# Kernel optimization log

Measured on AMD Instinct MI355X. Metric: run time of the kernel, lower is better.

The kernel has to match this reference:

```python
import jax, jax.numpy as jnp
import numpy as np

B, H, S, D = 2048, 1024, 32768, 64  # batch, hidden_dim, memory_slots, slot_size


def setup_inputs() -> dict:
    key = jax.random.key(0)
    ks = jax.random.split(key, 8)
    inp = {
        "query": jax.random.normal(ks[0], (B, H), jnp.float32),
        "consciousness_level": jax.random.uniform(ks[1], (B,), jnp.float32),
        "content": jax.random.normal(ks[2], (B, H), jnp.float32),
        "memory": jax.random.normal(ks[3], (S, D), jnp.float32) * 0.1,
        "memory_age": jnp.zeros((S,), jnp.float32),
        "memory_strength": jnp.ones((S,), jnp.float32) * 0.1,
        "W_read": jax.random.normal(ks[4], (H + 1, S), jnp.float32) / np.sqrt(H + 1),
        "b_read": jnp.zeros((S,), jnp.float32),
        "W_write": jax.random.normal(ks[5], (H + 1, S), jnp.float32) / np.sqrt(H + 1),
        "b_write": jnp.zeros((S,), jnp.float32),
        "W_cp": jax.random.normal(ks[6], (H, D), jnp.float32) / np.sqrt(H),
        "b_cp": jnp.zeros((D,), jnp.float32),
        "W_ce": jax.random.normal(ks[7], (D, H), jnp.float32) / np.sqrt(D),
        "b_ce": jnp.zeros((H,), jnp.float32),
    }
    return inp


def reference(query, consciousness_level, content, memory, memory_age,
              memory_strength, W_read, b_read, W_write, b_write,
              W_cp, b_cp, W_ce, b_ce):
    # ---- read path ----
    enhanced_query = jnp.concatenate([query, consciousness_level[:, None]], axis=-1)  # [B, H+1]
    read_weights = jax.nn.softmax(enhanced_query @ W_read + b_read, axis=-1)          # [B, S]
    boosted = read_weights * memory_strength[None, :]
    boosted = boosted / (boosted.sum(axis=-1, keepdims=True) + 1e-6)
    read_content = boosted @ memory                                                   # [B, D]
    consciousness_boost = read_content @ W_ce + b_ce                                  # [B, H]

    # ---- write path (vectorized masked consolidation over all slots) ----
    c_mean = consciousness_level.mean()
    write_weights = jax.nn.softmax(enhanced_query @ W_write + b_write, axis=-1)       # [B, S]
    ww_mean = write_weights.mean(axis=0)                                              # [S]
    pc_mean = (content @ W_cp + b_cp).mean(axis=0)                                    # [D]
    weight = ww_mean * (c_mean * 2.0)                                                 # [S]
    gate = c_mean >= 0.3                                                              # auto-activation threshold
    mask = (weight > 0.005) & gate                                                    # [S] bool
    consolidation = jax.nn.sigmoid(memory_age * 0.1 + c_mean)                         # [S]
    alpha = weight * consolidation                                                    # [S]
    new_memory = jnp.where(mask[:, None],
                           (1.0 - alpha)[:, None] * memory + alpha[:, None] * pc_mean[None, :],
                           memory)                                                    # [S, D]
    new_age = memory_age + mask.astype(memory_age.dtype)
    new_strength = jnp.where(mask,
                             jnp.clip(memory_strength + weight * 0.1, 0.1, 2.0),
                             memory_strength)
    return read_content, consciousness_boost, new_memory, new_age, new_strength
```

## Files before the change

kernel.cpp:

```cpp
#include <hip/hip_runtime.h>
#include <hip/hip_bf16.h>
#include <cstdint>
#include <cstddef>

#define B_ 2048
#define H_ 1024
#define S_ 32768
#define D_ 64
#define BT 32
#define KQ 1024
#define NT 16

typedef unsigned char u8;
typedef unsigned short u16;
typedef __attribute__((ext_vector_type(8))) short bf16x8;
typedef __attribute__((ext_vector_type(8))) unsigned short ushort8v;
typedef __attribute__((ext_vector_type(4))) float f32x4;

#define WS_CMEAN      0
#define WS_PCMEAN     64
#define WS_CMM        128
#define WS_ZR         (WS_CMM + H_)
#define WS_TR         (WS_ZR + B_)
#define WS_VR         (WS_TR + B_)
#define WS_ZW         (WS_VR + B_*D_)
#define WS_WWM        (WS_ZW + B_)
#define WS_END        (WS_WWM + S_)

__device__ __forceinline__ u16 f2bf(float f) {
  unsigned u = __float_as_uint(f);
  unsigned r = (u + 0x7FFFu + ((u >> 16) & 1u)) >> 16;
  return (u16)r;
}

__device__ __forceinline__ float bf2f(u16 v) {
  return __uint_as_float(((unsigned)v) << 16);
}

__device__ __forceinline__ u8 f8enc(float f) {
  f = fminf(f, 448.f);
  unsigned u = __float_as_uint(f);
  int ex = (int)((u >> 23) & 255) - 127;
  unsigned r;
  if (ex >= -6) {
    unsigned m = u & 0x7FFFFF;
    unsigned rm = (m + 0x7FFFF + ((m >> 20) & 1)) >> 20;
    r = ((unsigned)(ex + 7) << 3) + rm;
  } else {
    r = (unsigned)fminf(7.f, f * 512.f + 0.5f);
  }
  return (u8)(r > 126 ? 126 : r);
}

__device__ __forceinline__ float f8dec(u8 b) {
  int ef = (b >> 3) & 15, m = b & 7;
  return ef ? __uint_as_float(((unsigned)(ef + 120) << 23) | ((unsigned)m << 20))
            : (float)m * 0.001953125f;
}

__device__ __forceinline__ void gload_lds16(const void* g, void* l) {
  __builtin_amdgcn_global_load_lds(
      (const __attribute__((address_space(1))) unsigned int*)g,
      (__attribute__((address_space(3))) unsigned int*)l, 16, 0, 0);
}


__global__ void k_pre(const float* __restrict__ query, const float* __restrict__ cl,
                      const float* __restrict__ content, const float* __restrict__ mem,
                      const float* __restrict__ Wr, const float* __restrict__ Ww,
                      u16* __restrict__ qb, u16* __restrict__ mT,
                      u16* __restrict__ wbtR, u16* __restrict__ wbtW,
                      float* __restrict__ ws) {
  const int blk = blockIdx.x, t = threadIdx.x;
  if (blk < 128) {
    const int h = (blk & 3) * 256 + t;
    const int b0 = (blk >> 2) * 64;
    float acc = 0.f;
    #pragma unroll 8
    for (int b = 0; b < 64; ++b) acc += content[(size_t)(b0 + b) * H_ + h];
    atomicAdd(&ws[WS_CMM + h], acc * (1.0f / B_));
  } else if (blk < 160) {
    if (t < 64) {
      float acc = cl[(blk - 128) * 64 + t];
      #pragma unroll
      for (int off = 32; off > 0; off >>= 1) acc += __shfl_down(acc, off);
      if (t == 0) atomicAdd(&ws[WS_CMEAN], acc * (1.0f / B_));
    }
  } else if (blk < 160 + B_) {
    const int b = blk - 160;
    const float4 q4 = *reinterpret_cast<const float4*>(&query[(size_t)b * H_ + t * 4]);
    ushort4 o;
    o.x = f2bf(q4.x); o.y = f2bf(q4.y); o.z = f2bf(q4.z); o.w = f2bf(q4.w);
    *reinterpret_cast<ushort4*>(&qb[(size_t)b * KQ + t * 4]) = o;
  } else if (blk < 160 + B_ + 512) {
    __shared__ float tile[64][65];
    const int s0 = (blk - 160 - B_) * 64;
    const int c = t & 63, rbase = t >> 6;
    #pragma unroll
    for (int i = 0; i < 16; ++i) {
      const int r = rbase + i * 4;
      tile[r][c] = mem[(size_t)(s0 + r) * D_ + c];
    }
    __syncthreads();
    #pragma unroll
    for (int i = 0; i < 16; ++i) {
      const int d = rbase + i * 4;
      mT[(size_t)d * S_ + s0 + c] = f2bf(tile[c][d]);
    }
  } else {
    const int base = 160 + B_ + 512;
    const int isW = blk >= base + 8192;
    const int i = blk - base - (isW ? 8192 : 0);
    const float* __restrict__ W = isW ? Ww : Wr;
    u16* __restrict__ wbt = isW ? wbtW : wbtR;
    __shared__ float tile[64][65];
    const int s0 = (i & 511) * 64;
    const int k0 = (i >> 9) * 64;
    const int c = t & 63, rbase = t >> 6;
    #pragma unroll
    for (int j = 0; j < 16; ++j) {
      const int r = rbase + j * 4;
      tile[r][c] = W[(size_t)(k0 + r) * S_ + s0 + c];
    }
    __syncthreads();
    const int c8 = (t & 7) * 8;
    const int sr0 = t >> 3;
    #pragma unroll
    for (int j2 = 0; j2 < 2; ++j2) {
      const int srow = sr0 + 32 * j2;
      ushort8v o8;
      #pragma unroll
      for (int q = 0; q < 8; ++q) o8[q] = f2bf(tile[c8 + q][srow]);
      *reinterpret_cast<ushort8v*>(&wbt[(size_t)(s0 + srow) * KQ + k0 + c8]) = o8;
    }
  }
}

template <int NF>
__device__ __forceinline__ void rd_frags(const u16* __restrict__ lds, int rowbase,
                                         int lr, int lg, bf16x8 (&dst)[NF * 2]) {
  #pragma unroll
  for (int f = 0; f < NF; ++f) {
    const int rr = rowbase + f * 16 + lr;
    #pragma unroll
    for (int ks = 0; ks < 2; ++ks) {
      const int ch = (ks * 4 + lg) ^ (rr & 7);
      dst[f * 2 + ks] = *(const bf16x8*)&lds[rr * 64 + ch * 8];
    }
  }
}

template <int QR, int QC>
__device__ __forceinline__ void mfmaq(f32x4 (&acc)[8][4], const bf16x8 (&av)[8],
                                      const bf16x8 (&bv)[4]) {
  #pragma unroll
  for (int m16 = 0; m16 < 4; ++m16)
    #pragma unroll
    for (int n16 = 0; n16 < 2; ++n16)
      #pragma unroll
      for (int ks = 0; ks < 2; ++ks)
        acc[QR * 4 + m16][QC * 2 + n16] = __builtin_amdgcn_mfma_f32_16x16x32_bf16(
            av[m16 * 2 + ks], bv[n16 * 2 + ks], acc[QR * 4 + m16][QC * 2 + n16], 0, 0, 0);
}

template <int VARIANT>
__global__ __launch_bounds__(512, 2) void k_gemm(
    const u16* __restrict__ qb, const u16* __restrict__ wbt,
    const float* __restrict__ Wfull, const float* __restrict__ biasv,
    const float* __restrict__ cl, const float* __restrict__ strength,
    const u16* __restrict__ mT, void* __restrict__ pout, float* __restrict__ ws) {
  __shared__ __align__(16) u16 SMEM[4][256 * 64];
  const int t = threadIdx.x;
  const int w = t >> 6, l = t & 63;
  const int wm = w >> 2, wn = w & 3;
  const int lr = l & 15, lg = l >> 4;

  const int lin = blockIdx.x + 8 * blockIdx.y;
  const int xcd = lin & 7, idx = lin >> 3;
  const size_t r0 = (size_t)(idx & 7) * 256;
  const int cblk = xcd * 16 + (idx >> 3);
  const size_t c0 = (size_t)cblk * 256;

  f32x4 acc[8][4];
  #pragma unroll
  for (int m = 0; m < 8; ++m)
    #pragma unroll
    for (int n = 0; n < 4; ++n) acc[m][n] = (f32x4)0.f;

  auto STAGE = [&](int kt2, int pp) {
    #pragma unroll
    for (int i = 0; i < 4; ++i) {
      const int q = i * 512 + t;
      const int r = q >> 3;
      const int sc = (q & 7) ^ (r & 7);
      gload_lds16(qb + (r0 + r) * KQ + (size_t)kt2 * 64 + sc * 8, &SMEM[pp][q * 8]);
    }
    #pragma unroll
    for (int i = 0; i < 4; ++i) {
      const int q = i * 512 + t;
      const int r = q >> 3;
      const int sc = (q & 7) ^ (r & 7);
      gload_lds16(wbt + (c0 + r) * KQ + (size_t)kt2 * 64 + sc * 8, &SMEM[2 + pp][q * 8]);
    }
  };

  STAGE(0, 0);
  STAGE(1, 1);
  asm volatile("s_waitcnt vmcnt(8)" ::: "memory");
  __builtin_amdgcn_sched_barrier(0);
  __builtin_amdgcn_s_barrier();

  for (int kt = 0; kt < NT; ++kt) {
    const int p = kt & 1;
    const u16* __restrict__ Ap = &SMEM[p][0];
    const u16* __restrict__ Bp = &SMEM[2 + p][0];
    bf16x8 a[8], b0[4], b1[4];
    rd_frags<4>(Ap, wm * 128 + 0, lr, lg, a);
    rd_frags<2>(Bp, wn * 64 + 0, lr, lg, b0);
    __builtin_amdgcn_sched_barrier(0);
    __builtin_amdgcn_s_barrier();
    __builtin_amdgcn_s_setprio(1);
    mfmaq<0, 0>(acc, a, b0);
    __builtin_amdgcn_s_setprio(0);
    __builtin_amdgcn_s_barrier();
    rd_frags<2>(Bp, wn * 64 + 32, lr, lg, b1);
    __builtin_amdgcn_sched_barrier(0);
    __builtin_amdgcn_s_barrier();
    __builtin_amdgcn_s_setprio(1);
    mfmaq<0, 1>(acc, a, b1);
    __builtin_amdgcn_s_setprio(0);
    __builtin_amdgcn_s_barrier();
    rd_frags<4>(Ap, wm * 128 + 64, lr, lg, a);
    __builtin_amdgcn_sched_barrier(0);
    __builtin_amdgcn_s_barrier();
    __builtin_amdgcn_s_setprio(1);
    mfmaq<1, 1>(acc, a, b1);
    __builtin_amdgcn_s_setprio(0);
    __builtin_amdgcn_s_barrier();
    if (kt + 2 < NT) STAGE(kt + 2, p);
    __builtin_amdgcn_s_barrier();
    __builtin_amdgcn_s_setprio(1);
    mfmaq<1, 0>(acc, a, b0);
    __builtin_amdgcn_s_setprio(0);
    if (kt + 2 < NT) {
      asm volatile("s_waitcnt vmcnt(8)" ::: "memory");
    } else if (kt + 1 < NT) {
      asm volatile("s_waitcnt vmcnt(0)" ::: "memory");
    }
    __builtin_amdgcn_sched_barrier(0);
    __builtin_amdgcn_s_barrier();
  }

  float wl4[4], bb4[4];
  #pragma unroll
  for (int n = 0; n < 4; ++n) {
    const size_t col = c0 + wn * 64 + n * 16 + lr;
    wl4[n] = Wfull[(size_t)H_ * S_ + col];
    bb4[n] = biasv[col];
  }
  #pragma unroll
  for (int m = 0; m < 8; ++m) {
    #pragma unroll
    for (int j = 0; j < 4; ++j) {
      const float clv = cl[r0 + wm * 128 + m * 16 + lg * 4 + j];
      #pragma unroll
      for (int n = 0; n < 4; ++n)
        acc[m][n][j] += fmaf(clv, wl4[n], bb4[n]);
    }
  }

  u16* __restrict__ Plds = &SMEM[0][0];

  if (VARIANT == 0) {
    float st4[4];
    #pragma unroll
    for (int n = 0; n < 4; ++n) st4[n] = strength[c0 + wn * 64 + n * 16 + lr];
    #pragma unroll
    for (int m = 0; m < 8; ++m) {
      #pragma unroll
      for (int j = 0; j < 4; ++j) {
        const int rloc = wm * 128 + m * 16 + lg * 4 + j;
        float ze = 0.f, zp = 0.f;
        #pragma unroll
        for (int n = 0; n < 4; ++n) {
          const float e = __expf(acc[m][n][j]);
          const float pq = e * st4[n];
          ze += e;
          zp += pq;
          const int col = wn * 64 + n * 16 + lr;
          const int ch = (col >> 3) ^ (rloc & 7);
          Plds[rloc * 256 + ch * 8 + (col & 7)] = f2bf(pq);
        }
        #pragma unroll
        for (int off = 1; off < 16; off <<= 1) {
          ze += __shfl_xor(ze, off);
          zp += __shfl_xor(zp, off);
        }
        if (lr == 0) {
          atomicAdd(&ws[WS_ZR + r0 + rloc], ze);
          atomicAdd(&ws[WS_TR + r0 + rloc], zp);
        }
      }
    }
    __syncthreads();
    float* __restrict__ vp = (float*)pout;
    f32x4 pv[2][4];
    #pragma unroll
    for (int f = 0; f < 2; ++f)
      #pragma unroll
      for (int n = 0; n < 4; ++n) pv[f][n] = (f32x4)0.f;
    #pragma unroll 2
    for (int ks = 0; ks < 8; ++ks) {
      bf16x8 pa[2], pb[4];
      #pragma unroll
      for (int f = 0; f < 2; ++f) {
        const int row = w * 32 + f * 16 + lr;
        const int ch = (ks * 4 + lg) ^ (row & 7);
        pa[f] = *(const bf16x8*)&Plds[row * 256 + ch * 8];
      }
      #pragma unroll
      for (int n = 0; n < 4; ++n)
        pb[n] = *(const bf16x8*)&mT[(size_t)(n * 16 + lr) * S_ + c0 + ks * 32 + lg * 8];
      #pragma unroll
      for (int f = 0; f < 2; ++f)
        #pragma unroll
        for (int n = 0; n < 4; ++n)
          pv[f][n] = __builtin_amdgcn_mfma_f32_16x16x32_bf16(pa[f], pb[n], pv[f][n], 0, 0, 0);
    }
    #pragma unroll
    for (int f = 0; f < 2; ++f) {
      #pragma unroll
      for (int j = 0; j < 4; ++j) {
        const size_t R = (size_t)cblk * B_ + r0 + w * 32 + f * 16 + lg * 4 + j;
        #pragma unroll
        for (int n = 0; n < 4; ++n)
          vp[R * 64 + n * 16 + lr] = pv[f][n][j];
      }
    }
  } else {
    #pragma unroll
    for (int m = 0; m < 8; ++m) {
      #pragma unroll
      for (int j = 0; j < 4; ++j) {
        const int rloc = wm * 128 + m * 16 + lg * 4 + j;
        #pragma unroll
        for (int n = 0; n < 4; ++n) {
          const int col = wn * 64 + n * 16 + lr;
          const int ch = (col >> 3) ^ (rloc & 7);
          Plds[rloc * 256 + ch * 8 + (col & 7)] = f2bf(__expf(acc[m][n][j]));
        }
      }
    }
    __syncthreads();
    u8* __restrict__ pout8 = (u8*)pout;
    #pragma unroll 2
    for (int it = 0; it < 8; ++it) {
      const int row = w * 32 + it * 4 + (l >> 4);
      const int c2 = (l & 15) * 2;
      const bf16x8 e0 = *(const bf16x8*)&Plds[row * 256 + ((c2 ^ (row & 7)) * 8)];
      const bf16x8 e1 = *(const bf16x8*)&Plds[row * 256 + (((c2 + 1) ^ (row & 7)) * 8)];
      float ze = 0.f;
      uint4 fb;
      unsigned wds[4] = {0, 0, 0, 0};
      #pragma unroll
      for (int q = 0; q < 8; ++q) {
        const float ea = bf2f((u16)e0[q]);
        const float eb = bf2f((u16)e1[q]);
        ze += ea + eb;
        wds[q >> 2] |= ((unsigned)f8enc(ea)) << ((q & 3) * 8);
        wds[2 + (q >> 2)] |= ((unsigned)f8enc(eb)) << ((q & 3) * 8);
      }
      fb.x = wds[0]; fb.y = wds[1]; fb.z = wds[2]; fb.w = wds[3];
      *(uint4*)&pout8[(r0 + row) * S_ + c0 + (size_t)(l & 15) * 16] = fb;
      #pragma unroll
      for (int off = 1; off < 16; off <<= 1) ze += __shfl_xor(ze, off);
      if ((l & 15) == 0) atomicAdd(&ws[WS_ZW + r0 + row], ze);
    }
  }
}

__global__ void k_rc2cb(const float* __restrict__ vp, const float* __restrict__ Wcp,
                        const float* __restrict__ bcp, const float* __restrict__ Wce,
                        const float* __restrict__ bce, float* __restrict__ ws,
                        float* __restrict__ out_rc, float* __restrict__ out_cb) {
  const int t = threadIdx.x;
  if (blockIdx.x == 512) {
    __shared__ float red[4][64];
    const int d = t & 63, kk = t >> 6;
    float acc = 0.f;
    #pragma unroll 8
    for (int k = kk * 256; k < kk * 256 + 256; ++k)
      acc = fmaf(ws[WS_CMM + k], Wcp[(size_t)k * D_ + d], acc);
    red[kk][d] = acc;
    __syncthreads();
    if (t < 64) {
      float a = bcp[t];
      #pragma unroll
      for (int i = 0; i < 4; ++i) a += red[i][t];
      ws[WS_PCMEAN + t] = a;
    }
    return;
  }
  __shared__ float rcs[4][64];
  const int idx = blockIdx.x * 256 + t;
  const int b = idx >> 6, d = idx & 63;
  float v = 0.f;
  #pragma unroll 4
  for (int c = 0; c < 128; ++c) v += vp[(size_t)c * B_ * 64 + idx];
  const float rcv = v / (ws[WS_TR + b] + 1e-6f * ws[WS_ZR + b]);
  out_rc[idx] = rcv;
  rcs[t >> 6][d] = rcv;
  __syncthreads();
  const int b0 = blockIdx.x * 4;
  #pragma unroll
  for (int oo = 0; oo < 4; ++oo) {
    const int h = oo * 256 + t;
    float a0 = bce[h], a1 = a0, a2 = a0, a3 = a0;
    #pragma unroll 8
    for (int dd = 0; dd < 64; ++dd) {
      const float wv = Wce[(size_t)dd * H_ + h];
      a0 = fmaf(rcs[0][dd], wv, a0);
      a1 = fmaf(rcs[1][dd], wv, a1);
      a2 = fmaf(rcs[2][dd], wv, a2);
      a3 = fmaf(rcs[3][dd], wv, a3);
    }
    out_cb[(size_t)(b0 + 0) * H_ + h] = a0;
    out_cb[(size_t)(b0 + 1) * H_ + h] = a1;
    out_cb[(size_t)(b0 + 2) * H_ + h] = a2;
    out_cb[(size_t)(b0 + 3) * H_ + h] = a3;
  }
}


__global__ void k_wwm_f8(const u8* __restrict__ ebuf, float* __restrict__ ws) {
  const int t = threadIdx.x;
  const int s0 = blockIdx.x * 4096 + t * 16;
  const int b0 = blockIdx.y * 128;
  float ww[16];
  #pragma unroll
  for (int j = 0; j < 16; ++j) ww[j] = 0.f;
  #pragma unroll 1
  for (int b = 0; b < 128; ++b) {
    const float inv = 1.0f / ws[WS_ZW + b0 + b];
    const uint4 v = *reinterpret_cast<const uint4*>(&ebuf[(size_t)(b0 + b) * S_ + s0]);
    const unsigned vv[4] = {v.x, v.y, v.z, v.w};
    #pragma unroll
    for (int j = 0; j < 16; ++j) {
      const u8 byte = (u8)((vv[j >> 2] >> ((j & 3) * 8)) & 0xFF);
      ww[j] = fmaf(f8dec(byte), inv, ww[j]);
    }
  }
  #pragma unroll
  for (int j = 0; j < 16; ++j) atomicAdd(&ws[WS_WWM + s0 + j], ww[j]);
}

__global__ void k_final(const float* __restrict__ mem, const float* __restrict__ age,
                        const float* __restrict__ strength, const float* __restrict__ ws,
                        float* __restrict__ out_mem, float* __restrict__ out_age,
                        float* __restrict__ out_str) {
  const int idx = blockIdx.x * 256 + threadIdx.x;
  const int s = idx >> 6, dd = idx & 63;
  const float cm = ws[WS_CMEAN];
  const float w = ws[WS_WWM + s] * (2.0f * cm / B_);
  const bool mask = (w > 0.005f) && (cm >= 0.3f);
  float m = mem[idx];
  if (mask) {
    const float cons = 1.0f / (1.0f + __expf(-(age[s] * 0.1f + cm)));
    const float alpha = w * cons;
    m = (1.0f - alpha) * m + alpha * ws[WS_PCMEAN + dd];
  }
  out_mem[idx] = m;
  if (dd == 0) {
    out_age[s] = age[s] + (mask ? 1.0f : 0.0f);
    out_str[s] = mask ? fminf(fmaxf(strength[s] + w * 0.1f, 0.1f), 2.0f) : strength[s];
  }
}


__global__ void k_stats(const float* __restrict__ content,
                        const float* __restrict__ cl, float* __restrict__ ws) {
  const int gx = blockIdx.x, gy = blockIdx.y, t = threadIdx.x;
  if (gx < 4) {
    const int h = gx * 256 + t;
    const int b0 = gy * 64;
    float acc = 0.f;
    #pragma unroll 8
    for (int b = 0; b < 64; ++b) acc += content[(size_t)(b0 + b) * H_ + h];
    atomicAdd(&ws[WS_CMM + h], acc * (1.0f / B_));
  } else if (t < 64) {
    float acc = cl[gy * 64 + t];
    #pragma unroll
    for (int off = 32; off > 0; off >>= 1) acc += __shfl_down(acc, off);
    if (t == 0) atomicAdd(&ws[WS_CMEAN], acc * (1.0f / B_));
  }
}

__global__ void k_pcmean(const float* __restrict__ Wcp, const float* __restrict__ bcp,
                         float* __restrict__ ws) {
  __shared__ float red[16][64];
  const int t = threadIdx.x, d = t & 63, kk = t >> 6;
  float acc = 0.f;
  const int k0 = kk * 64;
  #pragma unroll 8
  for (int k = k0; k < k0 + 64; ++k)
    acc = fmaf(ws[WS_CMM + k], Wcp[(size_t)k * D_ + d], acc);
  red[kk][d] = acc;
  __syncthreads();
  if (t < 64) {
    float a = bcp[t];
    #pragma unroll
    for (int i = 0; i < 16; ++i) a += red[i][t];
    ws[WS_PCMEAN + t] = a;
  }
}

template <int NR>
__device__ __forceinline__ void logits_kloop(const float* __restrict__ q, int row0,
                                             const float* __restrict__ W, int s,
                                             float* acc) {
  #pragma unroll 1
  for (int k = 0; k < H_; k += 4) {
    const float w0 = W[(size_t)(k + 0) * S_ + s];
    const float w1 = W[(size_t)(k + 1) * S_ + s];
    const float w2 = W[(size_t)(k + 2) * S_ + s];
    const float w3 = W[(size_t)(k + 3) * S_ + s];
    #pragma unroll
    for (int r = 0; r < NR; ++r) {
      const float4 qv = *reinterpret_cast<const float4*>(&q[(size_t)(row0 + r) * H_ + k]);
      float a = acc[r];
      a = fmaf(qv.x, w0, a);
      a = fmaf(qv.y, w1, a);
      a = fmaf(qv.z, w2, a);
      a = fmaf(qv.w, w3, a);
      acc[r] = a;
    }
  }
}

__global__ __launch_bounds__(512, 2) void k_read(
    const float* __restrict__ q, const float* __restrict__ cl,
    const float* __restrict__ Wr, const float* __restrict__ br,
    const float* __restrict__ strength, const float* __restrict__ mem,
    float* __restrict__ ws) {
  __shared__ float plds[BT * 512];
  const int t = threadIdx.x;
  const int r0 = blockIdx.x * BT;
  const int squar = blockIdx.y;
  const int d = t & 63, wv = t >> 6;

  float zacc[BT], tacc[BT];
  #pragma unroll
  for (int r = 0; r < BT; ++r) { zacc[r] = 0.f; tacc[r] = 0.f; }
  float vacc[4] = {0.f, 0.f, 0.f, 0.f};

  for (int tile = 0; tile < 16; ++tile) {
    const int sg0 = squar * 8192 + tile * 512;
    const int s = sg0 + t;
    float acc[BT];
    const float wlast = Wr[(size_t)H_ * S_ + s];
    const float bias = br[s];
    #pragma unroll
    for (int r = 0; r < BT; ++r) acc[r] = fmaf(cl[r0 + r], wlast, bias);
    logits_kloop<BT>(q, r0, Wr, s, acc);

    const float stg = strength[s];
    #pragma unroll
    for (int r = 0; r < BT; ++r) {
      const float e = __expf(acc[r]);
      zacc[r] += e;
      const float p = e * stg;
      tacc[r] += p;
      plds[r * 512 + t] = p;
    }
    __syncthreads();
    #pragma unroll 1
    for (int sl = 0; sl < 512; sl += 4) {
      const float m0 = mem[(size_t)(sg0 + sl + 0) * D_ + d];
      const float m1 = mem[(size_t)(sg0 + sl + 1) * D_ + d];
      const float m2 = mem[(size_t)(sg0 + sl + 2) * D_ + d];
      const float m3 = mem[(size_t)(sg0 + sl + 3) * D_ + d];
      #pragma unroll
      for (int j = 0; j < 4; ++j) {
        const float4 pv = *reinterpret_cast<const float4*>(&plds[(wv + 8 * j) * 512 + sl]);
        float v = vacc[j];
        v = fmaf(pv.x, m0, v);
        v = fmaf(pv.y, m1, v);
        v = fmaf(pv.z, m2, v);
        v = fmaf(pv.w, m3, v);
        vacc[j] = v;
      }
    }
    __syncthreads();
  }

  float* red0 = plds;
  float* red1 = plds + 8 * BT;
  #pragma unroll
  for (int r = 0; r < BT; ++r) {
    float z = zacc[r], tt = tacc[r];
    #pragma unroll
    for (int off = 32; off > 0; off >>= 1) {
      z += __shfl_down(z, off);
      tt += __shfl_down(tt, off);
    }
    if ((t & 63) == 0) { red0[wv * BT + r] = z; red1[wv * BT + r] = tt; }
  }
  __syncthreads();
  if (t < BT) {
    float z = 0.f, tt = 0.f;
    #pragma unroll
    for (int wq = 0; wq < 8; ++wq) { z += red0[wq * BT + t]; tt += red1[wq * BT + t]; }
    atomicAdd(&ws[WS_ZR + r0 + t], z);
    atomicAdd(&ws[WS_TR + r0 + t], tt);
  }
  #pragma unroll
  for (int j = 0; j < 4; ++j)
    atomicAdd(&ws[WS_VR + (size_t)(r0 + wv + 8 * j) * D_ + d], vacc[j]);
}

__global__ __launch_bounds__(512, 2) void k_write_pass1(
    const float* __restrict__ q, const float* __restrict__ cl,
    const float* __restrict__ Ww, const float* __restrict__ bw,
    float* __restrict__ ws, __hip_bfloat16* __restrict__ ebuf, const int store_e) {
  __shared__ float red[8 * BT];
  const int t = threadIdx.x;
  const int r0 = blockIdx.x * BT;
  const int squar = blockIdx.y;
  const int wv = t >> 6;

  float zacc[BT];
  #pragma unroll
  for (int r = 0; r < BT; ++r) zacc[r] = 0.f;

  for (int tile = 0; tile < 16; ++tile) {
    const int s = squar * 8192 + tile * 512 + t;
    float acc[BT];
    const float wlast = Ww[(size_t)H_ * S_ + s];
    const float bias = bw[s];
    #pragma unroll
    for (int r = 0; r < BT; ++r) acc[r] = fmaf(cl[r0 + r], wlast, bias);
    logits_kloop<BT>(q, r0, Ww, s, acc);
    #pragma unroll
    for (int r = 0; r < BT; ++r) {
      const float e = __expf(acc[r]);
      zacc[r] += e;
      if (store_e) ebuf[(size_t)(r0 + r) * S_ + s] = __float2bfloat16(e);
    }
  }
  #pragma unroll
  for (int r = 0; r < BT; ++r) {
    float z = zacc[r];
    #pragma unroll
    for (int off = 32; off > 0; off >>= 1) z += __shfl_down(z, off);
    if ((t & 63) == 0) red[wv * BT + r] = z;
  }
  __syncthreads();
  if (t < BT) {
    float z = 0.f;
    #pragma unroll
    for (int wq = 0; wq < 8; ++wq) z += red[wq * BT + t];
    atomicAdd(&ws[WS_ZW + r0 + t], z);
  }
}

__global__ void k_rc(const float* __restrict__ ws, float* __restrict__ out) {
  const int idx = blockIdx.x * 256 + threadIdx.x;
  const int b = idx >> 6;
  const float z = ws[WS_ZR + b], tt = ws[WS_TR + b];
  out[idx] = ws[WS_VR + idx] / (tt + 1e-6f * z);
}

__global__ void k_cboost(const float* __restrict__ rc, const float* __restrict__ Wce,
                         const float* __restrict__ bce, float* __restrict__ out) {
  const int idx = blockIdx.x * 256 + threadIdx.x;
  const int b = idx >> 10, h = idx & 1023;
  const float* __restrict__ rcb = &rc[b * 64];
  float acc = bce[h];
  #pragma unroll
  for (int dd = 0; dd < 64; dd += 4) {
    const float4 r4 = *reinterpret_cast<const float4*>(&rcb[dd]);
    acc = fmaf(r4.x, Wce[(size_t)(dd + 0) * H_ + h], acc);
    acc = fmaf(r4.y, Wce[(size_t)(dd + 1) * H_ + h], acc);
    acc = fmaf(r4.z, Wce[(size_t)(dd + 2) * H_ + h], acc);
    acc = fmaf(r4.w, Wce[(size_t)(dd + 3) * H_ + h], acc);
  }
  out[idx] = acc;
}

__global__ void k_wwm_store(const __hip_bfloat16* __restrict__ ebuf,
                            float* __restrict__ ws) {
  const int t = threadIdx.x;
  const int s0 = blockIdx.x * 2048 + t * 8;
  const int b0 = blockIdx.y * 128;
  const u16* __restrict__ eb = (const u16*)ebuf;
  float ww[8];
  #pragma unroll
  for (int j = 0; j < 8; ++j) ww[j] = 0.f;
  #pragma unroll 1
  for (int b = 0; b < 128; ++b) {
    const float inv = 1.0f / ws[WS_ZW + b0 + b];
    const ushort8v ev = *reinterpret_cast<const ushort8v*>(&eb[(size_t)(b0 + b) * S_ + s0]);
    #pragma unroll
    for (int j = 0; j < 8; ++j) {
      const float e = __uint_as_float(((unsigned)ev[j]) << 16);
      ww[j] = fmaf(e, inv, ww[j]);
    }
  }
  #pragma unroll
  for (int j = 0; j < 8; ++j) atomicAdd(&ws[WS_WWM + s0 + j], ww[j]);
}

__global__ __launch_bounds__(512, 2) void k_wwm_recompute(
    const float* __restrict__ q, const float* __restrict__ cl,
    const float* __restrict__ Ww, const float* __restrict__ bw,
    float* __restrict__ ws) {
  const int t = threadIdx.x;
  const int s = blockIdx.x * 512 + t;
  const int b0 = blockIdx.y * 256;
  const float wlast = Ww[(size_t)H_ * S_ + s];
  const float bias = bw[s];
  float wwacc = 0.f;
  for (int g = 0; g < 8; ++g) {
    const int rb = b0 + g * 32;
    float acc[BT];
    #pragma unroll
    for (int r = 0; r < BT; ++r) acc[r] = fmaf(cl[rb + r], wlast, bias);
    logits_kloop<BT>(q, rb, Ww, s, acc);
    #pragma unroll
    for (int r = 0; r < BT; ++r) wwacc += __expf(acc[r]) / ws[WS_ZW + rb + r];
  }
  atomicAdd(&ws[WS_WWM + s], wwacc);
}


extern "C" void kernel_launch(void* const* d_in, const int* in_sizes, int n_in,
                              void* d_out, int out_size, void* d_ws, size_t ws_size,
                              hipStream_t stream) {
  const float* query    = (const float*)d_in[0];
  const float* cl       = (const float*)d_in[1];
  const float* content  = (const float*)d_in[2];
  const float* memory   = (const float*)d_in[3];
  const float* age      = (const float*)d_in[4];
  const float* strength = (const float*)d_in[5];
  const float* W_read   = (const float*)d_in[6];
  const float* b_read   = (const float*)d_in[7];
  const float* W_write  = (const float*)d_in[8];
  const float* b_write  = (const float*)d_in[9];
  const float* W_cp     = (const float*)d_in[10];
  const float* b_cp     = (const float*)d_in[11];
  const float* W_ce     = (const float*)d_in[12];
  const float* b_ce     = (const float*)d_in[13];

  float* out = (float*)d_out;
  float* ws = (float*)d_ws;
  float* out_rc  = out;
  float* out_cb  = out + B_ * D_;
  float* out_mem = out_cb + (size_t)B_ * H_;
  float* out_age = out_mem + (size_t)S_ * D_;
  float* out_str = out_age + S_;

  const size_t QB_F    = WS_END;
  const size_t MEMT_F  = QB_F + (size_t)B_ * KQ / 2;
  const size_t WBTR_F  = MEMT_F + (size_t)D_ * S_ / 2;
  const size_t WBTW_F  = WBTR_F + (size_t)S_ * KQ / 2;
  const size_t PBUF_F  = WBTW_F + (size_t)S_ * KQ / 2;
  const size_t FAST_END_F = PBUF_F + (size_t)128 * B_ * 64;

  hipMemsetAsync(ws, 0, (size_t)WS_END * sizeof(float), stream);

  if (ws_size >= FAST_END_F * sizeof(float)) {
    u16* qb   = (u16*)(ws + QB_F);
    u16* mT   = (u16*)(ws + MEMT_F);
    u16* wbtR = (u16*)(ws + WBTR_F);
    u16* wbtW = (u16*)(ws + WBTW_F);
    float* vp = (float*)(ws + PBUF_F);
    u8*  pf8  = (u8*)(ws + PBUF_F);

    k_pre<<<160 + B_ + 512 + 2 * 8192, 256, 0, stream>>>(
        query, cl, content, memory, W_read, W_write, qb, mT, wbtR, wbtW, ws);
    k_gemm<0><<<dim3(8, 128), 512, 0, stream>>>(qb, wbtR, W_read, b_read, cl,
                                                strength, mT, (void*)vp, ws);
    k_rc2cb<<<513, 256, 0, stream>>>(vp, W_cp, b_cp, W_ce, b_ce, ws, out_rc, out_cb);
    k_gemm<1><<<dim3(8, 128), 512, 0, stream>>>(qb, wbtW, W_write, b_write, cl,
                                                nullptr, mT, (void*)pf8, ws);
    k_wwm_f8<<<dim3(8, 16), 256, 0, stream>>>(pf8, ws);
    k_final<<<(S_ * D_) / 256, 256, 0, stream>>>(memory, age, strength, ws,
                                                 out_mem, out_age, out_str);
  } else {
    const size_t ebuf_bytes = (size_t)B_ * S_ * 2;
    const int store_e = (ws_size >= (size_t)WS_END * 4 + ebuf_bytes) ? 1 : 0;
    __hip_bfloat16* ebuf = (__hip_bfloat16*)(ws + WS_END);

    k_stats<<<dim3(5, 32), 256, 0, stream>>>(content, cl, ws);
    k_pcmean<<<1, 1024, 0, stream>>>(W_cp, b_cp, ws);
    k_read<<<dim3(B_ / BT, 4), 512, 0, stream>>>(query, cl, W_read, b_read, strength, memory, ws);
    k_write_pass1<<<dim3(B_ / BT, 4), 512, 0, stream>>>(query, cl, W_write, b_write, ws, ebuf, store_e);
    k_rc<<<(B_ * D_) / 256, 256, 0, stream>>>(ws, out_rc);
    k_cboost<<<(B_ * H_) / 256, 256, 0, stream>>>(out_rc, W_ce, b_ce, out_cb);
    if (store_e) {
      k_wwm_store<<<dim3(S_ / 2048, B_ / 128), 256, 0, stream>>>(ebuf, ws);
    } else {
      k_wwm_recompute<<<dim3(S_ / 512, 8), 512, 0, stream>>>(query, cl, W_write, b_write, ws);
    }
    k_final<<<(S_ * D_) / 256, 256, 0, stream>>>(memory, age, strength, ws,
                                                 out_mem, out_age, out_str);
  }
}
```

Measured before the change: 673.4 us.

## Merge read and write GEMM kernels into one launch with separate output buffers

Refactors the GEMM into a device body and adds a merged kernel whose grid covers both the read-path and write-path GEMMs, choosing the variant by block index. The write path's fp8 buffer gets its own workspace region so it no longer aliases the read-path partials. The aim is to remove one launch and the tail or serialization gap between the two large GEMMs so both fill the GPU together. It needs more workspace, and falls back to the old path when the workspace is too small.

Measured after the change: 662.1 us. No clear change (-1.7%).

```diff
diff --git a/kernel.cpp b/kernel.cpp
--- a/kernel.cpp
+++ b/kernel.cpp
@@ -163,19 +163,24 @@
             av[m16 * 2 + ks], bv[n16 * 2 + ks], acc[QR * 4 + m16][QC * 2 + n16], 0, 0, 0);
 }
 
-template <int VARIANT>
-__global__ __launch_bounds__(512, 2) void k_gemm(
+template <int IS_MERGED, int TVARIANT>
+__device__ __forceinline__ void gemm_body(
+    u16* __restrict__ SMEM, int variant, int bx, int by,
     const u16* __restrict__ qb, const u16* __restrict__ wbt,
     const float* __restrict__ Wfull, const float* __restrict__ biasv,
     const float* __restrict__ cl, const float* __restrict__ strength,
     const u16* __restrict__ mT, void* __restrict__ pout, float* __restrict__ ws) {
-  __shared__ __align__(16) u16 SMEM[4][256 * 64];
   const int t = threadIdx.x;
   const int w = t >> 6, l = t & 63;
   const int wm = w >> 2, wn = w & 3;
   const int lr = l & 15, lg = l >> 4;
 
-  const int lin = blockIdx.x + 8 * blockIdx.y;
+  u16* __restrict__ SA0 = SMEM;
+  u16* __restrict__ SA1 = SMEM + 256 * 64;
+  u16* __restrict__ SB0 = SMEM + 2 * 256 * 64;
+  u16* __restrict__ SB1 = SMEM + 3 * 256 * 64;
+
+  const int lin = bx + 8 * by;
   const int xcd = lin & 7, idx = lin >> 3;
   const size_t r0 = (size_t)(idx & 7) * 256;
   const int cblk = xcd * 16 + (idx >> 3);
@@ -188,19 +193,21 @@
     for (int n = 0; n < 4; ++n) acc[m][n] = (f32x4)0.f;
 
   auto STAGE = [&](int kt2, int pp) {
+    u16* __restrict__ SA = pp ? SA1 : SA0;
+    u16* __restrict__ SB = pp ? SB1 : SB0;
     #pragma unroll
     for (int i = 0; i < 4; ++i) {
       const int q = i * 512 + t;
       const int r = q >> 3;
       const int sc = (q & 7) ^ (r & 7);
-      gload_lds16(qb + (r0 + r) * KQ + (size_t)kt2 * 64 + sc * 8, &SMEM[pp][q * 8]);
+      gload_lds16(qb + (r0 + r) * KQ + (size_t)kt2 * 64 + sc * 8, &SA[q * 8]);
     }
     #pragma unroll
     for (int i = 0; i < 4; ++i) {
       const int q = i * 512 + t;
       const int r = q >> 3;
       const int sc = (q & 7) ^ (r & 7);
-      gload_lds16(wbt + (c0 + r) * KQ + (size_t)kt2 * 64 + sc * 8, &SMEM[2 + pp][q * 8]);
+      gload_lds16(wbt + (c0 + r) * KQ + (size_t)kt2 * 64 + sc * 8, &SB[q * 8]);
     }
   };
 
@@ -212,8 +219,8 @@
 
   for (int kt = 0; kt < NT; ++kt) {
     const int p = kt & 1;
-    const u16* __restrict__ Ap = &SMEM[p][0];
-    const u16* __restrict__ Bp = &SMEM[2 + p][0];
+    const u16* __restrict__ Ap = p ? SA1 : SA0;
+    const u16* __restrict__ Bp = p ? SB1 : SB0;
     bf16x8 a[8], b0[4], b1[4];
     rd_frags<4>(Ap, wm * 128 + 0, lr, lg, a);
     rd_frags<2>(Bp, wn * 64 + 0, lr, lg, b0);
@@ -269,9 +276,10 @@
     }
   }
 
-  u16* __restrict__ Plds = &SMEM[0][0];
-
-  if (VARIANT == 0) {
+  u16* __restrict__ Plds = SMEM;
+
+  const int v = IS_MERGED ? variant : TVARIANT;
+  if (v == 0) {
     float st4[4];
     #pragma unroll
     for (int n = 0; n < 4; ++n) st4[n] = strength[c0 + wn * 64 + n * 16 + lr];
@@ -379,6 +387,36 @@
   }
 }
 
+template <int VARIANT>
+__global__ __launch_bounds__(512, 2) void k_gemm(
+    const u16* __restrict__ qb, const u16* __restrict__ wbt,
+    const float* __restrict__ Wfull, const float* __restrict__ biasv,
+    const float* __restrict__ cl, const float* __restrict__ strength,
+    const u16* __restrict__ mT, void* __restrict__ pout, float* __restrict__ ws) {
+  __shared__ __align__(16) u16 SMEM[4 * 256 * 64];
+  gemm_body<0, VARIANT>(SMEM, VARIANT, blockIdx.x, blockIdx.y, qb, wbt, Wfull,
+                        biasv, cl, strength, mT, pout, ws);
+}
+
+__global__ __launch_bounds__(512, 2) void k_gemm2(
+    const u16* __restrict__ qb, const u16* __restrict__ wbtR,
+    const u16* __restrict__ wbtW,
+    const float* __restrict__ Wr, const float* __restrict__ br,
+    const float* __restrict__ Ww, const float* __restrict__ bw,
+    const float* __restrict__ cl, const float* __restrict__ strength,
+    const u16* __restrict__ mT, void* __restrict__ vp, void* __restrict__ pf8,
+    float* __restrict__ ws) {
+  __shared__ __align__(16) u16 SMEM[4 * 256 * 64];
+  const int variant = (blockIdx.y >= 128) ? 1 : 0;
+  const int by = blockIdx.y & 127;
+  if (variant == 0)
+    gemm_body<1, 0>(SMEM, 0, blockIdx.x, by, qb, wbtR, Wr, br, cl, strength,
+                    mT, vp, ws);
+  else
+    gemm_body<1, 1>(SMEM, 1, blockIdx.x, by, qb, wbtW, Ww, bw, cl, strength,
+                    mT, pf8, ws);
+}
+
 __global__ void k_rc2cb(const float* __restrict__ vp, const float* __restrict__ Wcp,
                         const float* __restrict__ bcp, const float* __restrict__ Wce,
                         const float* __restrict__ bce, float* __restrict__ ws,
@@ -764,11 +802,31 @@
   const size_t WBTR_F  = MEMT_F + (size_t)D_ * S_ / 2;
   const size_t WBTW_F  = WBTR_F + (size_t)S_ * KQ / 2;
   const size_t PBUF_F  = WBTW_F + (size_t)S_ * KQ / 2;
-  const size_t FAST_END_F = PBUF_F + (size_t)128 * B_ * 64;
+  const size_t VPN_F   = PBUF_F;
+  const size_t PF8N_F  = PBUF_F + (size_t)128 * B_ * 64;
+  const size_t FAST1_END_F = PBUF_F + (size_t)128 * B_ * 64;
+  const size_t FAST2_END_F = PF8N_F + (size_t)B_ * S_ / 4;
 
   hipMemsetAsync(ws, 0, (size_t)WS_END * sizeof(float), stream);
 
-  if (ws_size >= FAST_END_F * sizeof(float)) {
+  if (ws_size >= FAST2_END_F * sizeof(float)) {
+    u16* qb   = (u16*)(ws + QB_F);
+    u16* mT   = (u16*)(ws + MEMT_F);
+    u16* wbtR = (u16*)(ws + WBTR_F);
+    u16* wbtW = (u16*)(ws + WBTW_F);
+    float* vp = (float*)(ws + VPN_F);
+    u8*  pf8  = (u8*)(ws + PF8N_F);
+
+    k_pre<<<160 + B_ + 512 + 2 * 8192, 256, 0, stream>>>(
+        query, cl, content, memory, W_read, W_write, qb, mT, wbtR, wbtW, ws);
+    k_gemm2<<<dim3(8, 256), 512, 0, stream>>>(qb, wbtR, wbtW, W_read, b_read,
+                                              W_write, b_write, cl, strength,
+                                              mT, (void*)vp, (void*)pf8, ws);
+    k_rc2cb<<<513, 256, 0, stream>>>(vp, W_cp, b_cp, W_ce, b_ce, ws, out_rc, out_cb);
+    k_wwm_f8<<<dim3(8, 16), 256, 0, stream>>>(pf8, ws);
+    k_final<<<(S_ * D_) / 256, 256, 0, stream>>>(memory, age, strength, ws,
+                                                 out_mem, out_age, out_str);
+  } else if (ws_size >= FAST1_END_F * sizeof(float)) {
     u16* qb   = (u16*)(ws + QB_F);
     u16* mT   = (u16*)(ws + MEMT_F);
     u16* wbtR = (u16*)(ws + WBTR_F);
```
